# Performance work log

Hardware: AMD Instinct MI355X
Metric: run time of the kernel (lower is better)

The kernel has to match this reference:

```python
import jax, jax.numpy as jnp
import numpy as np

DIM = 1024
HEADS = 16
HEAD_DIM = DIM // HEADS
MAX_REL = 1024
B, N = 4, 1024


def setup_inputs() -> dict:
    key = jax.random.key(0)
    k1, k2, k3, k4, k5 = jax.random.split(key, 5)
    x = jax.random.normal(k1, (B, N, DIM), dtype=jnp.float32)
    W_qkv = jax.random.normal(k2, (3 * DIM, DIM), dtype=jnp.float32) * 0.02
    W_proj = jax.random.normal(k3, (DIM, DIM), dtype=jnp.float32) * 0.02
    b_proj = jnp.zeros((DIM,), dtype=jnp.float32)
    Er = jax.random.normal(k4, (MAX_REL, HEAD_DIM), dtype=jnp.float32)
    return {"x": x, "W_qkv": W_qkv, "W_proj": W_proj, "b_proj": b_proj, "Er": Er}


def _relative_skew(S_rel):
    # S_rel: [B, H, L, L] -> pad a zero column on the left, reshape, drop first row
    Bb, H, L, _ = S_rel.shape
    S = jnp.pad(S_rel, ((0, 0), (0, 0), (0, 0), (1, 0)))  # [B,H,L,L+1]
    S = S.reshape(Bb, H, L + 1, L)
    return S[:, :, 1:, :]


def reference(x, W_qkv, W_proj, b_proj, Er):
    Bb, Nn, C = x.shape
    scale = HEAD_DIM ** (-0.5)
    qkv = jnp.einsum('bnc,fc->bnf', x, W_qkv)           # [B,N,3C]
    qkv = qkv.reshape(Bb, Nn, 3, HEADS, HEAD_DIM)
    q = jnp.transpose(qkv[:, :, 0], (0, 2, 1, 3))        # [B,H,N,d]
    k = jnp.transpose(qkv[:, :, 1], (0, 2, 1, 3))
    v = jnp.transpose(qkv[:, :, 2], (0, 2, 1, 3))
    content = jnp.einsum('bhnd,bhmd->bhnm', q, k)        # [B,H,N,N]
    er_seq = Er[:Nn]                                     # [N,d]
    rel = jnp.einsum('bhnd,md->bhnm', q, er_seq)         # [B,H,N,N]
    rel = _relative_skew(rel)
    score = (content + rel) * scale
    causal = jnp.triu(jnp.ones((Nn, Nn), dtype=bool), k=1)
    score = jnp.where(causal, -jnp.inf, score)
    probs = jax.nn.softmax(score, axis=-1)
    out = jnp.einsum('bhnm,bhmd->bhnd', probs, v)        # [B,H,N,d]
    out = jnp.transpose(out, (0, 2, 1, 3)).reshape(Bb, Nn, C)
    return jnp.einsum('bnc,oc->bno', out, W_proj) + b_proj
```

## Files before the change

### kernel.cpp

```cpp
#include <hip/hip_runtime.h>
#include <math.h>

#define BATCH 4
#define SEQ   1024
#define DIM_C 1024
#define HEADS 16
#define HDIM  64
#define F3    3072

typedef short bf8 __attribute__((ext_vector_type(8)));
typedef float f32x4 __attribute__((ext_vector_type(4)));

__device__ __forceinline__ ushort f2bf(float f) {
    union { float f; unsigned u; } c; c.f = f;
    unsigned u = c.u + 0x7fffu + ((c.u >> 16) & 1u);
    return (ushort)(u >> 16);
}
__device__ __forceinline__ float bf2f(ushort s) {
    union { unsigned u; float f; } c; c.u = ((unsigned)s) << 16;
    return c.f;
}

__device__ __forceinline__ void stage16(const ushort* g, ushort* l) {
    __builtin_amdgcn_global_load_lds(
        (const __attribute__((address_space(1))) unsigned int*)g,
        (__attribute__((address_space(3))) unsigned int*)l, 16, 0, 0);
}

__global__ __launch_bounds__(256) void cvt_all_kernel(
    const float* __restrict__ x, const float* __restrict__ wqkv,
    const float* __restrict__ wproj, const float* __restrict__ er,
    ushort* __restrict__ xb, ushort* __restrict__ wqkvb,
    ushort* __restrict__ wprojb, ushort* __restrict__ erb)
{
    const int blk = blockIdx.x;
    const float* src; ushort* dst; size_t off;
    if (blk < 2048)      { src = x;     dst = xb;     off = (size_t)blk * 2048; }
    else if (blk < 3584) { src = wqkv;  dst = wqkvb;  off = (size_t)(blk - 2048) * 2048; }
    else if (blk < 4096) { src = wproj; dst = wprojb; off = (size_t)(blk - 3584) * 2048; }
    else                 { src = er;    dst = erb;    off = (size_t)(blk - 4096) * 2048; }
    size_t i = off + (size_t)threadIdx.x * 8;
    float4 v0 = *(const float4*)&src[i];
    float4 v1 = *(const float4*)&src[i + 4];
    ushort o[8];
    o[0] = f2bf(v0.x); o[1] = f2bf(v0.y); o[2] = f2bf(v0.z); o[3] = f2bf(v0.w);
    o[4] = f2bf(v1.x); o[5] = f2bf(v1.y); o[6] = f2bf(v1.z); o[7] = f2bf(v1.w);
    *(uint4*)&dst[i] = *(uint4*)o;
}

__device__ __forceinline__ void gemm_core(
    const ushort* __restrict__ a, const ushort* __restrict__ b,
    ushort* As, ushort* Bs, int m0, int f0, int t, f32x4 (&acc)[4][4])
{
    const int lane = t & 63, w = t >> 6;
    const int lc = lane & 15, g4 = lane >> 4;
    const int wm = (w >> 1) * 64, wn = (w & 1) * 64;
    const int rowS = w * 32 + (lane >> 2);
    const int kkS  = (lane & 3) * 8;

    for (int kt = 0; kt < 32; ++kt) {
        const int k0 = kt * 32;
        __syncthreads();
        #pragma unroll
        for (int ii = 0; ii < 2; ++ii) {
            stage16(&a[(size_t)(m0 + rowS + ii * 16) * 1024 + k0 + kkS],
                    &As[(w * 2 + ii) * 512]);
            stage16(&b[(size_t)(f0 + rowS + ii * 16) * 1024 + k0 + kkS],
                    &Bs[(w * 2 + ii) * 512]);
        }
        __syncthreads();
        bf8 af[4], bfr[4];
        #pragma unroll
        for (int mb = 0; mb < 4; ++mb)
            af[mb] = *(const bf8*)&As[(wm + mb * 16 + lc) * 32 + g4 * 8];
        #pragma unroll
        for (int nb = 0; nb < 4; ++nb)
            bfr[nb] = *(const bf8*)&Bs[(wn + nb * 16 + lc) * 32 + g4 * 8];
        #pragma unroll
        for (int mb = 0; mb < 4; ++mb)
            #pragma unroll
            for (int nb = 0; nb < 4; ++nb)
                acc[mb][nb] = __builtin_amdgcn_mfma_f32_16x16x32_bf16(
                    af[mb], bfr[nb], acc[mb][nb], 0, 0, 0);
    }
}

__global__ __launch_bounds__(256) void gemm_qkv_mfma(
    const ushort* __restrict__ xb, const ushort* __restrict__ wb,
    ushort* __restrict__ qp, ushort* __restrict__ kp, ushort* __restrict__ vp)
{
    __shared__ __align__(16) ushort As[128 * 32];
    __shared__ __align__(16) ushort Bs[128 * 32];
    const int t = threadIdx.x;
    const int m0 = blockIdx.y * 128, f0 = blockIdx.x * 128;
    f32x4 acc[4][4];
    #pragma unroll
    for (int mb = 0; mb < 4; ++mb)
        #pragma unroll
        for (int nb = 0; nb < 4; ++nb) acc[mb][nb] = (f32x4){0.f, 0.f, 0.f, 0.f};

    gemm_core(xb, wb, As, Bs, m0, f0, t, acc);

    const int lane = t & 63, w = t >> 6;
    const int lc = lane & 15, g4 = lane >> 4;
    const int wm = (w >> 1) * 64, wn = (w & 1) * 64;
    const int s = f0 >> 10;
    #pragma unroll
    for (int mb = 0; mb < 4; ++mb)
        #pragma unroll
        for (int nb = 0; nb < 4; ++nb) {
            const int f = f0 + wn + nb * 16 + lc;
            const int h = (f >> 6) & 15, d = f & 63;
            if (s == 2) {
                const int m = m0 + wm + mb * 16 + g4 * 4;
                const int b = m >> 10, n = m & 1023;
                ushort4 o;
                o.x = f2bf(acc[mb][nb][0]); o.y = f2bf(acc[mb][nb][1]);
                o.z = f2bf(acc[mb][nb][2]); o.w = f2bf(acc[mb][nb][3]);
                *(ushort4*)&vp[(((size_t)(b * 16 + h)) * 64 + d) * 1024 + n] = o;
            } else {
                ushort* dst = (s == 0) ? qp : kp;
                #pragma unroll
                for (int i = 0; i < 4; ++i) {
                    const int m = m0 + wm + mb * 16 + g4 * 4 + i;
                    const int b = m >> 10, n = m & 1023;
                    dst[(((size_t)(b * 16 + h)) * 1024 + n) * 64 + d] = f2bf(acc[mb][nb][i]);
                }
            }
        }
}

__global__ __launch_bounds__(256) void gemm_proj_mfma(
    const ushort* __restrict__ ab, const ushort* __restrict__ wb,
    const float* __restrict__ bias, float* __restrict__ y)
{
    __shared__ __align__(16) ushort As[128 * 32];
    __shared__ __align__(16) ushort Bs[128 * 32];
    const int t = threadIdx.x;
    const int m0 = blockIdx.y * 128, f0 = blockIdx.x * 128;
    f32x4 acc[4][4];
    #pragma unroll
    for (int mb = 0; mb < 4; ++mb)
        #pragma unroll
        for (int nb = 0; nb < 4; ++nb) acc[mb][nb] = (f32x4){0.f, 0.f, 0.f, 0.f};

    gemm_core(ab, wb, As, Bs, m0, f0, t, acc);

    const int lane = t & 63, w = t >> 6;
    const int lc = lane & 15, g4 = lane >> 4;
    const int wm = (w >> 1) * 64, wn = (w & 1) * 64;
    #pragma unroll
    for (int mb = 0; mb < 4; ++mb)
        #pragma unroll
        for (int nb = 0; nb < 4; ++nb) {
            const int f = f0 + wn + nb * 16 + lc;
            const float bv = bias[f];
            #pragma unroll
            for (int i = 0; i < 4; ++i) {
                const int m = m0 + wm + mb * 16 + g4 * 4 + i;
                y[(size_t)m * 1024 + f] = acc[mb][nb][i] + bv;
            }
        }
}

__global__ __launch_bounds__(256, 3) void attn_mfma_kernel(
    const ushort* __restrict__ qg, const ushort* __restrict__ kg,
    const ushort* __restrict__ vtg, const ushort* __restrict__ erg,
    ushort* __restrict__ pOd, float* __restrict__ pL)
{
    __shared__ __align__(16) ushort k_s[2][64][64];
    __shared__ __align__(16) ushort vt_s[2][64][64];
    __shared__ __align__(16) ushort r_s[4][16][80];
    __shared__ __align__(16) ushort p_s[4][16][72];

    const int t = threadIdx.x;
    const int w = t >> 6, lane = t & 63;
    const int lc = lane & 15, g4 = lane >> 4;
    const int b = blockIdx.z, h = blockIdx.y;
    const int u = blockIdx.x;
    const int cum[17] = {0,1,2,3,4,6,8,10,12,15,18,21,24,28,32,36,40};
    int bx = 0;
    #pragma unroll
    for (int j = 1; j < 16; ++j) if (u >= cum[j]) bx = j;
    const int part = u - cum[bx];
    const int t0 = part * 4;
    const int t1 = min(t0 + 4, bx + 1);

    const int n0 = bx * 64;
    const int n0w = n0 + w * 16;
    const int eB0 = 960 - n0;
    const int ew0 = 48 - 16 * w;

    const ushort* qb  = qg  + ((size_t)(b * 16 + h)) * 65536;
    const ushort* kb  = kg  + ((size_t)(b * 16 + h)) * 65536;
    const ushort* vtb = vtg + ((size_t)(b * 16 + h)) * 65536;

    const int srow = lane >> 3;
    const int scol = ((lane & 7) ^ (srow & 7)) * 8;
    const int sr0  = w * 16 + srow;
    const int rsw  = (lc & 7) * 8;

    #pragma unroll
    for (int ii = 0; ii < 2; ++ii) {
        stage16(&kb[(size_t)(t0 * 64 + sr0 + ii * 8) * 64 + scol], &k_s[0][w * 16 + ii * 8][0]);
        stage16(&vtb[(size_t)(sr0 + ii * 8) * 1024 + t0 * 64 + scol], &vt_s[0][w * 16 + ii * 8][0]);
    }

    bf8 qf[2];
    #pragma unroll
    for (int c = 0; c < 2; ++c)
        qf[c] = *(const bf8*)&qb[(size_t)(n0w + lc) * 64 + c * 32 + g4 * 8];

    asm volatile("s_waitcnt vmcnt(0)" ::: "memory");
    __builtin_amdgcn_s_barrier();

    const f32x4 z4 = {0.f, 0.f, 0.f, 0.f};
    f32x4 od[4] = {z4, z4, z4, z4};
    float lrow[4] = {0.f, 0.f, 0.f, 0.f};
    int cur = 0;

    for (int tt = t0; tt < t1; ++tt) {
        const int m0 = tt * 64;
        const int eB = eB0 + m0;

        if (tt + 1 < t1) {
            const int m1 = m0 + 64;
            const int nxt = cur ^ 1;
            #pragma unroll
            for (int ii = 0; ii < 2; ++ii) {
                stage16(&kb[(size_t)(m1 + sr0 + ii * 8) * 64 + scol],
                        &k_s[nxt][w * 16 + ii * 8][0]);
                stage16(&vtb[(size_t)(sr0 + ii * 8) * 1024 + m1 + scol],
                        &vt_s[nxt][w * 16 + ii * 8][0]);
            }
            asm volatile("s_waitcnt vmcnt(4)" ::: "memory");
        } else {
            asm volatile("s_waitcnt vmcnt(0)" ::: "memory");
        }
        __builtin_amdgcn_s_barrier();

        bf8 ef[5][2];
        #pragma unroll
        for (int jr = 0; jr < 5; ++jr) {
            int row = eB + ew0 + jr * 16 + lc;
            row = (row > 1023) ? 1023 : row;
            #pragma unroll
            for (int c = 0; c < 2; ++c)
                ef[jr][c] = *(const bf8*)&erg[(size_t)row * 64 + c * 32 + g4 * 8];
        }

        f32x4 sc[4] = {z4, z4, z4, z4};
        #pragma unroll
        for (int jt = 0; jt < 4; ++jt)
            #pragma unroll
            for (int c = 0; c < 2; ++c) {
                bf8 kf = *(const bf8*)&k_s[cur][jt * 16 + lc][((c * 4 + g4) * 8) ^ rsw];
                sc[jt] = __builtin_amdgcn_mfma_f32_16x16x32_bf16(qf[c], kf, sc[jt], 0, 0, 0);
            }

        f32x4 rc[5] = {z4, z4, z4, z4, z4};
        #pragma unroll
        for (int jr = 0; jr < 5; ++jr)
            #pragma unroll
            for (int c = 0; c < 2; ++c)
                rc[jr] = __builtin_amdgcn_mfma_f32_16x16x32_bf16(qf[c], ef[jr][c], rc[jr], 0, 0, 0);

        #pragma unroll
        for (int jr = 0; jr < 5; ++jr)
            #pragma unroll
            for (int i = 0; i < 4; ++i)
                r_s[w][g4 * 4 + i][jr * 16 + lc] = f2bf(rc[jr][i]);
        asm volatile("s_waitcnt lgkmcnt(0)" ::: "memory");

        #pragma unroll
        for (int i = 0; i < 4; ++i) {
            const int row = g4 * 4 + i;
            const int n = n0w + row;
            #pragma unroll
            for (int jt = 0; jt < 4; ++jt) {
                const int colR = jt * 16 + lc + 15 - row;
                const float rel = bf2f(r_s[w][row][colR]);
                const float s = (sc[jt][i] + rel) * 0.125f;
                const int m = m0 + jt * 16 + lc;
                const float p = (m <= n) ? __expf(s) : 0.f;
                p_s[w][row][jt * 16 + lc] = f2bf(p);
                lrow[i] += p;
            }
        }
        asm volatile("s_waitcnt lgkmcnt(0)" ::: "memory");

        bf8 pf[2];
        #pragma unroll
        for (int c = 0; c < 2; ++c)
            pf[c] = *(const bf8*)&p_s[w][lc][c * 32 + g4 * 8];
        #pragma unroll
        for (int dt = 0; dt < 4; ++dt)
            #pragma unroll
            for (int c = 0; c < 2; ++c) {
                bf8 vf = *(const bf8*)&vt_s[cur][dt * 16 + lc][((c * 4 + g4) * 8) ^ rsw];
                od[dt] = __builtin_amdgcn_mfma_f32_16x16x32_bf16(pf[c], vf, od[dt], 0, 0, 0);
            }

        __builtin_amdgcn_s_barrier();
        cur ^= 1;
    }

    #pragma unroll
    for (int off = 1; off < 16; off <<= 1)
        #pragma unroll
        for (int i = 0; i < 4; ++i)
            lrow[i] += __shfl_xor(lrow[i], off, 16);

    const size_t pbase = (size_t)((b * 16 + h) * 40 + u);
    #pragma unroll
    for (int i = 0; i < 4; ++i) {
        const int nl = w * 16 + g4 * 4 + i;
        #pragma unroll
        for (int dt = 0; dt < 4; ++dt)
            pOd[pbase * 4096 + nl * 64 + dt * 16 + lc] = f2bf(od[dt][i]);
        if (lc == 0) pL[pbase * 64 + nl] = lrow[i];
    }
}

__global__ __launch_bounds__(256) void attn_combine_kernel(
    const ushort* __restrict__ pOd, const float* __restrict__ pL,
    ushort* __restrict__ attnb)
{
    const int tid = blockIdx.x * 256 + threadIdx.x;
    const int d8 = tid & 7;
    const int n  = (tid >> 3) & 1023;
    const int bh = tid >> 13;
    const int bx = n >> 6, nl = n & 63;
    const int cum[17] = {0,1,2,3,4,6,8,10,12,15,18,21,24,28,32,36,40};
    const int u0 = cum[bx], pc = cum[bx + 1] - cum[bx];

    float acc[8] = {0.f, 0.f, 0.f, 0.f, 0.f, 0.f, 0.f, 0.f};
    float lsum = 0.f;
    for (int j = 0; j < pc; ++j) {
        const size_t base = (size_t)(bh * 40 + u0 + j);
        uint4 pv = *(const uint4*)&pOd[base * 4096 + nl * 64 + d8 * 8];
        const ushort* pp = (const ushort*)&pv;
        #pragma unroll
        for (int e = 0; e < 8; ++e) acc[e] += bf2f(pp[e]);
        lsum += pL[base * 64 + nl];
    }
    const float inv = 1.f / lsum;
    ushort o[8];
    #pragma unroll
    for (int e = 0; e < 8; ++e) o[e] = f2bf(acc[e] * inv);
    const int b = bh >> 4, h = bh & 15;
    *(uint4*)&attnb[((size_t)(b * 1024) + n) * 1024 + h * 64 + d8 * 8] = *(uint4*)o;
}

extern "C" void kernel_launch(void* const* d_in, const int* in_sizes, int n_in,
                              void* d_out, int out_size, void* d_ws, size_t ws_size,
                              hipStream_t stream)
{
    const float* x     = (const float*)d_in[0];
    const float* Wqkv  = (const float*)d_in[1];
    const float* Wproj = (const float*)d_in[2];
    const float* bproj = (const float*)d_in[3];
    const float* Er    = (const float*)d_in[4];
    float* out = (float*)d_out;

    const size_t per = (size_t)BATCH * HEADS * SEQ * HDIM;
    ushort* xb     = (ushort*)d_ws;
    ushort* wqkvb  = xb + (size_t)4194304;
    ushort* wprojb = wqkvb + (size_t)3145728;
    ushort* erb    = wprojb + (size_t)1048576;
    ushort* qw     = erb + (size_t)65536;
    ushort* kw     = qw + per;
    ushort* vw     = kw + per;
    ushort* attnb  = vw + per;
    ushort* pOd    = attnb + per;
    float*  pL     = (float*)(pOd + (size_t)64 * 40 * 4096);

    cvt_all_kernel<<<dim3(4128), 256, 0, stream>>>(
        x, Wqkv, Wproj, Er, xb, wqkvb, wprojb, erb);

    gemm_qkv_mfma<<<dim3(F3 / 128, (BATCH * SEQ) / 128), 256, 0, stream>>>(
        xb, wqkvb, qw, kw, vw);

    attn_mfma_kernel<<<dim3(40, HEADS, BATCH), 256, 0, stream>>>(
        qw, kw, vw, erb, pOd, pL);

    attn_combine_kernel<<<dim3(2048), 256, 0, stream>>>(pOd, pL, attnb);

    gemm_proj_mfma<<<dim3(DIM_C / 128, (BATCH * SEQ) / 128), 256, 0, stream>>>(
        attnb, wprojb, bproj, out);
}
```

Measured before the change: 215.6 us.

## Stage relative-position Er chunks through a triple-buffered LDS ring

Er rows used by the relative-position MFMA were previously loaded straight from global memory into registers on every tile. They are now prefetched asynchronously into a three-slot LDS ring, loaded two chunks ahead, and read with the same swizzle used for K. This is meant to hide global-load latency and cut redundant global traffic. The cost is extra LDS (about 24KB more), and launch bounds drop from 3 to 2 blocks per SM, which may reduce occupancy. The r_s row padding also changes from 80 to 84.

```diff
diff --git a/kernel.cpp b/kernel.cpp
--- a/kernel.cpp
+++ b/kernel.cpp
@@ -163,14 +163,15 @@
         }
 }
 
-__global__ __launch_bounds__(256, 3) void attn_mfma_kernel(
+__global__ __launch_bounds__(256, 2) void attn_mfma_kernel(
     const ushort* __restrict__ qg, const ushort* __restrict__ kg,
     const ushort* __restrict__ vtg, const ushort* __restrict__ erg,
     ushort* __restrict__ pOd, float* __restrict__ pL)
 {
     __shared__ __align__(16) ushort k_s[2][64][64];
     __shared__ __align__(16) ushort vt_s[2][64][64];
-    __shared__ __align__(16) ushort r_s[4][16][80];
+    __shared__ __align__(16) ushort e_s[3][64][64];
+    __shared__ __align__(16) ushort r_s[4][16][84];
     __shared__ __align__(16) ushort p_s[4][16][72];
 
     const int t = threadIdx.x;
@@ -188,8 +189,8 @@
 
     const int n0 = bx * 64;
     const int n0w = n0 + w * 16;
-    const int eB0 = 960 - n0;
     const int ew0 = 48 - 16 * w;
+    const int ch0 = 15 - bx + t0;
 
     const ushort* qb  = qg  + ((size_t)(b * 16 + h)) * 65536;
     const ushort* kb  = kg  + ((size_t)(b * 16 + h)) * 65536;
@@ -205,6 +206,16 @@
         stage16(&kb[(size_t)(t0 * 64 + sr0 + ii * 8) * 64 + scol], &k_s[0][w * 16 + ii * 8][0]);
         stage16(&vtb[(size_t)(sr0 + ii * 8) * 1024 + t0 * 64 + scol], &vt_s[0][w * 16 + ii * 8][0]);
     }
+    #pragma unroll
+    for (int cc = 0; cc < 2; ++cc) {
+        const int ch = ch0 + cc;
+        #pragma unroll
+        for (int ii = 0; ii < 2; ++ii) {
+            int gr = ch * 64 + sr0 + ii * 8;
+            gr = (gr > 1023) ? 1023 : gr;
+            stage16(&erg[(size_t)gr * 64 + scol], &e_s[ch % 3][w * 16 + ii * 8][0]);
+        }
+    }
 
     bf8 qf[2];
     #pragma unroll
@@ -221,7 +232,8 @@
 
     for (int tt = t0; tt < t1; ++tt) {
         const int m0 = tt * 64;
-        const int eB = eB0 + m0;
+        const int ch = 15 - bx + tt;
+        const int eB = ch * 64;
 
         if (tt + 1 < t1) {
             const int m1 = m0 + 64;
@@ -233,21 +245,17 @@
                 stage16(&vtb[(size_t)(sr0 + ii * 8) * 1024 + m1 + scol],
                         &vt_s[nxt][w * 16 + ii * 8][0]);
             }
-            asm volatile("s_waitcnt vmcnt(4)" ::: "memory");
+            #pragma unroll
+            for (int ii = 0; ii < 2; ++ii) {
+                int gr = (ch + 2) * 64 + sr0 + ii * 8;
+                gr = (gr > 1023) ? 1023 : gr;
+                stage16(&erg[(size_t)gr * 64 + scol], &e_s[(ch + 2) % 3][w * 16 + ii * 8][0]);
+            }
+            asm volatile("s_waitcnt vmcnt(6)" ::: "memory");
         } else {
             asm volatile("s_waitcnt vmcnt(0)" ::: "memory");
         }
         __builtin_amdgcn_s_barrier();
-
-        bf8 ef[5][2];
-        #pragma unroll
-        for (int jr = 0; jr < 5; ++jr) {
-            int row = eB + ew0 + jr * 16 + lc;
-            row = (row > 1023) ? 1023 : row;
-            #pragma unroll
-            for (int c = 0; c < 2; ++c)
-                ef[jr][c] = *(const bf8*)&erg[(size_t)row * 64 + c * 32 + g4 * 8];
-        }
 
         f32x4 sc[4] = {z4, z4, z4, z4};
         #pragma unroll
@@ -260,10 +268,16 @@
 
         f32x4 rc[5] = {z4, z4, z4, z4, z4};
         #pragma unroll
-        for (int jr = 0; jr < 5; ++jr)
-            #pragma unroll
-            for (int c = 0; c < 2; ++c)
-                rc[jr] = __builtin_amdgcn_mfma_f32_16x16x32_bf16(qf[c], ef[jr][c], rc[jr], 0, 0, 0);
+        for (int jr = 0; jr < 5; ++jr) {
+            const int g  = eB + ew0 + jr * 16 + lc;
+            const int s3 = (g >> 6) % 3;
+            const int r  = g & 63;
+            #pragma unroll
+            for (int c = 0; c < 2; ++c) {
+                bf8 ef = *(const bf8*)&e_s[s3][r][((c * 4 + g4) * 8) ^ rsw];
+                rc[jr] = __builtin_amdgcn_mfma_f32_16x16x32_bf16(qf[c], ef, rc[jr], 0, 0, 0);
+            }
+        }
 
         #pragma unroll
         for (int jr = 0; jr < 5; ++jr)
```

New measurement: 209.2 us. 3.0% less time.

## Store Q/K/V/Er in MFMA-fragment order and load attention operands directly

Applied to the files above, without the earlier changes.

The QKV GEMM epilogue now writes Q, K and V in a pre-swizzled layout that matches the MFMA fragment order, and a new kernel packs Er the same way with zero-padded tiles. The attention kernel then drops its LDS double-buffering of K and V and the barriers, loading each fragment with one coalesced 16-byte global load per lane. The relative-score scratch is kept in fp32 instead of bf16. The aim is to remove LDS staging and synchronisation overhead, at the cost of scattered 2-byte stores in the GEMM epilogue and less latency hiding for the global loads.

```diff
diff --git a/kernel.cpp b/kernel.cpp
--- a/kernel.cpp
+++ b/kernel.cpp
@@ -29,16 +29,15 @@
 
 __global__ __launch_bounds__(256) void cvt_all_kernel(
     const float* __restrict__ x, const float* __restrict__ wqkv,
-    const float* __restrict__ wproj, const float* __restrict__ er,
+    const float* __restrict__ wproj,
     ushort* __restrict__ xb, ushort* __restrict__ wqkvb,
-    ushort* __restrict__ wprojb, ushort* __restrict__ erb)
+    ushort* __restrict__ wprojb)
 {
     const int blk = blockIdx.x;
     const float* src; ushort* dst; size_t off;
     if (blk < 2048)      { src = x;     dst = xb;     off = (size_t)blk * 2048; }
     else if (blk < 3584) { src = wqkv;  dst = wqkvb;  off = (size_t)(blk - 2048) * 2048; }
-    else if (blk < 4096) { src = wproj; dst = wprojb; off = (size_t)(blk - 3584) * 2048; }
-    else                 { src = er;    dst = erb;    off = (size_t)(blk - 4096) * 2048; }
+    else                 { src = wproj; dst = wprojb; off = (size_t)(blk - 3584) * 2048; }
     size_t i = off + (size_t)threadIdx.x * 8;
     float4 v0 = *(const float4*)&src[i];
     float4 v1 = *(const float4*)&src[i + 4];
@@ -48,6 +47,26 @@
     *(uint4*)&dst[i] = *(uint4*)o;
 }
 
+__global__ __launch_bounds__(256) void er_pack_kernel(
+    const float* __restrict__ er, ushort* __restrict__ erp)
+{
+    const int tid = blockIdx.x * 256 + threadIdx.x;
+    const int rt = tid >> 6, lane = tid & 63;
+    const int lc = lane & 15, g4 = lane >> 4;
+    const int row = rt * 16 + lc;
+    #pragma unroll
+    for (int c = 0; c < 2; ++c) {
+        ushort o[8] = {0, 0, 0, 0, 0, 0, 0, 0};
+        if (row < 1024) {
+            float4 a = *(const float4*)&er[(size_t)row * 64 + c * 32 + g4 * 8];
+            float4 q = *(const float4*)&er[(size_t)row * 64 + c * 32 + g4 * 8 + 4];
+            o[0] = f2bf(a.x); o[1] = f2bf(a.y); o[2] = f2bf(a.z); o[3] = f2bf(a.w);
+            o[4] = f2bf(q.x); o[5] = f2bf(q.y); o[6] = f2bf(q.z); o[7] = f2bf(q.w);
+        }
+        *(uint4*)&erp[(size_t)rt * 1024 + c * 512 + lane * 8] = *(uint4*)o;
+    }
+}
+
 __device__ __forceinline__ void gemm_core(
     const ushort* __restrict__ a, const ushort* __restrict__ b,
     ushort* As, ushort* Bs, int m0, int f0, int t, f32x4 (&acc)[4][4])
@@ -111,21 +130,21 @@
         for (int nb = 0; nb < 4; ++nb) {
             const int f = f0 + wn + nb * 16 + lc;
             const int h = (f >> 6) & 15, d = f & 63;
-            if (s == 2) {
-                const int m = m0 + wm + mb * 16 + g4 * 4;
+            #pragma unroll
+            for (int i = 0; i < 4; ++i) {
+                const int m = m0 + wm + mb * 16 + g4 * 4 + i;
                 const int b = m >> 10, n = m & 1023;
-                ushort4 o;
-                o.x = f2bf(acc[mb][nb][0]); o.y = f2bf(acc[mb][nb][1]);
-                o.z = f2bf(acc[mb][nb][2]); o.w = f2bf(acc[mb][nb][3]);
-                *(ushort4*)&vp[(((size_t)(b * 16 + h)) * 64 + d) * 1024 + n] = o;
-            } else {
-                ushort* dst = (s == 0) ? qp : kp;
-                #pragma unroll
-                for (int i = 0; i < 4; ++i) {
-                    const int m = m0 + wm + mb * 16 + g4 * 4 + i;
-                    const int b = m >> 10, n = m & 1023;
-                    dst[(((size_t)(b * 16 + h)) * 1024 + n) * 64 + d] = f2bf(acc[mb][nb][i]);
-                }
+                const size_t bho = (size_t)(b * 16 + h) * 65536;
+                const ushort val = f2bf(acc[mb][nb][i]);
+                if (s == 0)
+                    qp[bho + (n >> 4) * 1024 + (d >> 5) * 512 + ((d >> 3) & 3) * 128
+                           + (n & 15) * 8 + (d & 7)] = val;
+                else if (s == 1)
+                    kp[bho + (n >> 4) * 1024 + (d >> 5) * 512 + ((d >> 3) & 3) * 128
+                           + (n & 15) * 8 + (d & 7)] = val;
+                else
+                    vp[bho + (n >> 6) * 4096 + (d >> 4) * 1024 + ((n >> 5) & 1) * 512
+                           + ((n >> 3) & 3) * 128 + (d & 15) * 8 + (n & 7)] = val;
             }
         }
 }
@@ -164,13 +183,11 @@
 }
 
 __global__ __launch_bounds__(256, 3) void attn_mfma_kernel(
-    const ushort* __restrict__ qg, const ushort* __restrict__ kg,
-    const ushort* __restrict__ vtg, const ushort* __restrict__ erg,
+    const ushort* __restrict__ qp, const ushort* __restrict__ kp,
+    const ushort* __restrict__ vp, const ushort* __restrict__ erp,
     ushort* __restrict__ pOd, float* __restrict__ pL)
 {
-    __shared__ __align__(16) ushort k_s[2][64][64];
-    __shared__ __align__(16) ushort vt_s[2][64][64];
-    __shared__ __align__(16) ushort r_s[4][16][80];
+    __shared__ float r_s[4][16][84];
     __shared__ __align__(16) ushort p_s[4][16][72];
 
     const int t = threadIdx.x;
@@ -186,77 +203,44 @@
     const int t0 = part * 4;
     const int t1 = min(t0 + 4, bx + 1);
 
-    const int n0 = bx * 64;
-    const int n0w = n0 + w * 16;
-    const int eB0 = 960 - n0;
-    const int ew0 = 48 - 16 * w;
-
-    const ushort* qb  = qg  + ((size_t)(b * 16 + h)) * 65536;
-    const ushort* kb  = kg  + ((size_t)(b * 16 + h)) * 65536;
-    const ushort* vtb = vtg + ((size_t)(b * 16 + h)) * 65536;
-
-    const int srow = lane >> 3;
-    const int scol = ((lane & 7) ^ (srow & 7)) * 8;
-    const int sr0  = w * 16 + srow;
-    const int rsw  = (lc & 7) * 8;
-
-    #pragma unroll
-    for (int ii = 0; ii < 2; ++ii) {
-        stage16(&kb[(size_t)(t0 * 64 + sr0 + ii * 8) * 64 + scol], &k_s[0][w * 16 + ii * 8][0]);
-        stage16(&vtb[(size_t)(sr0 + ii * 8) * 1024 + t0 * 64 + scol], &vt_s[0][w * 16 + ii * 8][0]);
-    }
+    const int n0w = bx * 64 + w * 16;
+    const size_t bho = (size_t)(b * 16 + h) * 65536;
+    const ushort* qb = qp + bho;
+    const ushort* kb = kp + bho;
+    const ushort* vb = vp + bho;
 
     bf8 qf[2];
     #pragma unroll
     for (int c = 0; c < 2; ++c)
-        qf[c] = *(const bf8*)&qb[(size_t)(n0w + lc) * 64 + c * 32 + g4 * 8];
-
-    asm volatile("s_waitcnt vmcnt(0)" ::: "memory");
-    __builtin_amdgcn_s_barrier();
+        qf[c] = *(const bf8*)&qb[(size_t)(bx * 4 + w) * 1024 + c * 512 + lane * 8];
 
     const f32x4 z4 = {0.f, 0.f, 0.f, 0.f};
     f32x4 od[4] = {z4, z4, z4, z4};
     float lrow[4] = {0.f, 0.f, 0.f, 0.f};
-    int cur = 0;
 
     for (int tt = t0; tt < t1; ++tt) {
         const int m0 = tt * 64;
-        const int eB = eB0 + m0;
-
-        if (tt + 1 < t1) {
-            const int m1 = m0 + 64;
-            const int nxt = cur ^ 1;
-            #pragma unroll
-            for (int ii = 0; ii < 2; ++ii) {
-                stage16(&kb[(size_t)(m1 + sr0 + ii * 8) * 64 + scol],
-                        &k_s[nxt][w * 16 + ii * 8][0]);
-                stage16(&vtb[(size_t)(sr0 + ii * 8) * 1024 + m1 + scol],
-                        &vt_s[nxt][w * 16 + ii * 8][0]);
-            }
-            asm volatile("s_waitcnt vmcnt(4)" ::: "memory");
-        } else {
-            asm volatile("s_waitcnt vmcnt(0)" ::: "memory");
-        }
-        __builtin_amdgcn_s_barrier();
-
+        const int rte = (15 - bx + tt) * 4 + (3 - w);
+
+        bf8 kf[4][2];
+        #pragma unroll
+        for (int jt = 0; jt < 4; ++jt)
+            #pragma unroll
+            for (int c = 0; c < 2; ++c)
+                kf[jt][c] = *(const bf8*)&kb[(size_t)(tt * 4 + jt) * 1024 + c * 512 + lane * 8];
         bf8 ef[5][2];
         #pragma unroll
-        for (int jr = 0; jr < 5; ++jr) {
-            int row = eB + ew0 + jr * 16 + lc;
-            row = (row > 1023) ? 1023 : row;
-            #pragma unroll
-            for (int c = 0; c < 2; ++c)
-                ef[jr][c] = *(const bf8*)&erg[(size_t)row * 64 + c * 32 + g4 * 8];
-        }
+        for (int jr = 0; jr < 5; ++jr)
+            #pragma unroll
+            for (int c = 0; c < 2; ++c)
+                ef[jr][c] = *(const bf8*)&erp[(size_t)(rte + jr) * 1024 + c * 512 + lane * 8];
 
         f32x4 sc[4] = {z4, z4, z4, z4};
         #pragma unroll
         for (int jt = 0; jt < 4; ++jt)
             #pragma unroll
-            for (int c = 0; c < 2; ++c) {
-                bf8 kf = *(const bf8*)&k_s[cur][jt * 16 + lc][((c * 4 + g4) * 8) ^ rsw];
-                sc[jt] = __builtin_amdgcn_mfma_f32_16x16x32_bf16(qf[c], kf, sc[jt], 0, 0, 0);
-            }
+            for (int c = 0; c < 2; ++c)
+                sc[jt] = __builtin_amdgcn_mfma_f32_16x16x32_bf16(qf[c], kf[jt][c], sc[jt], 0, 0, 0);
 
         f32x4 rc[5] = {z4, z4, z4, z4, z4};
         #pragma unroll
@@ -265,11 +249,18 @@
             for (int c = 0; c < 2; ++c)
                 rc[jr] = __builtin_amdgcn_mfma_f32_16x16x32_bf16(qf[c], ef[jr][c], rc[jr], 0, 0, 0);
 
+        bf8 vf[4][2];
+        #pragma unroll
+        for (int dt = 0; dt < 4; ++dt)
+            #pragma unroll
+            for (int c = 0; c < 2; ++c)
+                vf[dt][c] = *(const bf8*)&vb[(size_t)(tt * 4096 + dt * 1024 + c * 512) + lane * 8];
+
         #pragma unroll
         for (int jr = 0; jr < 5; ++jr)
             #pragma unroll
             for (int i = 0; i < 4; ++i)
-                r_s[w][g4 * 4 + i][jr * 16 + lc] = f2bf(rc[jr][i]);
+                r_s[w][g4 * 4 + i][jr * 16 + lc] = rc[jr][i];
         asm volatile("s_waitcnt lgkmcnt(0)" ::: "memory");
 
         #pragma unroll
@@ -279,7 +270,7 @@
             #pragma unroll
             for (int jt = 0; jt < 4; ++jt) {
                 const int colR = jt * 16 + lc + 15 - row;
-                const float rel = bf2f(r_s[w][row][colR]);
+                const float rel = r_s[w][row][colR];
                 const float s = (sc[jt][i] + rel) * 0.125f;
                 const int m = m0 + jt * 16 + lc;
                 const float p = (m <= n) ? __expf(s) : 0.f;
@@ -296,13 +287,8 @@
         #pragma unroll
         for (int dt = 0; dt < 4; ++dt)
             #pragma unroll
-            for (int c = 0; c < 2; ++c) {
-                bf8 vf = *(const bf8*)&vt_s[cur][dt * 16 + lc][((c * 4 + g4) * 8) ^ rsw];
-                od[dt] = __builtin_amdgcn_mfma_f32_16x16x32_bf16(pf[c], vf, od[dt], 0, 0, 0);
-            }
-
-        __builtin_amdgcn_s_barrier();
-        cur ^= 1;
+            for (int c = 0; c < 2; ++c)
+                od[dt] = __builtin_amdgcn_mfma_f32_16x16x32_bf16(pf[c], vf[dt][c], od[dt], 0, 0, 0);
     }
 
     #pragma unroll
@@ -367,22 +353,24 @@
     ushort* xb     = (ushort*)d_ws;
     ushort* wqkvb  = xb + (size_t)4194304;
     ushort* wprojb = wqkvb + (size_t)3145728;
-    ushort* erb    = wprojb + (size_t)1048576;
-    ushort* qw     = erb + (size_t)65536;
+    ushort* erp    = wprojb + (size_t)1048576;
+    ushort* qw     = erp + (size_t)131072;
     ushort* kw     = qw + per;
     ushort* vw     = kw + per;
     ushort* attnb  = vw + per;
     ushort* pOd    = attnb + per;
     float*  pL     = (float*)(pOd + (size_t)64 * 40 * 4096);
 
-    cvt_all_kernel<<<dim3(4128), 256, 0, stream>>>(
-        x, Wqkv, Wproj, Er, xb, wqkvb, wprojb, erb);
+    cvt_all_kernel<<<dim3(4096), 256, 0, stream>>>(
+        x, Wqkv, Wproj, xb, wqkvb, wprojb);
+
+    er_pack_kernel<<<dim3(17), 256, 0, stream>>>(Er, erp);
 
     gemm_qkv_mfma<<<dim3(F3 / 128, (BATCH * SEQ) / 128), 256, 0, stream>>>(
         xb, wqkvb, qw, kw, vw);
 
     attn_mfma_kernel<<<dim3(40, HEADS, BATCH), 256, 0, stream>>>(
-        qw, kw, vw, erb, pOd, pL);
+        qw, kw, vw, erp, pOd, pL);
 
     attn_combine_kernel<<<dim3(2048), 256, 0, stream>>>(pOd, pL, attnb);
 
```

After: 212.7 us. About the same (-1.3%).
